# Kernel optimization log

Hardware: AMD Instinct MI355X
Metric: run time of the kernel (lower is better)

Reference implementation:

```python
import jax, jax.numpy as jnp
import numpy as np

N = 50000          # nodes
E = 800000         # edges (before self-loops)
IN_C = 128         # input feature dim
H = 4              # attention heads
C = 32             # channels per head (hidden == out == 32)
G = 64             # graphs in the batch
NEG_SLOPE_ATT = 0.2   # PyG GATConv default negative_slope
NEG_SLOPE_ACT = 0.01  # nn.LeakyReLU default


def setup_inputs() -> dict:
    key = jax.random.key(0)
    ks = jax.random.split(key, 16)
    x = jax.random.normal(ks[0], (N, IN_C), dtype=jnp.float32)
    edge_index = jax.random.randint(ks[1], (2, E), 0, N, dtype=jnp.int64)
    batch = jnp.sort(jax.random.randint(ks[2], (N,), 0, G, dtype=jnp.int64))
    def gat_params(k, din):
        k1, k2, k3 = jax.random.split(k, 3)
        W = jax.random.normal(k1, (din, H * C), dtype=jnp.float32) * (1.0 / np.sqrt(din))
        a_src = jax.random.normal(k2, (H, C), dtype=jnp.float32) * 0.1
        a_dst = jax.random.normal(k3, (H, C), dtype=jnp.float32) * 0.1
        b = jnp.zeros((H * C,), dtype=jnp.float32)
        return W, a_src, a_dst, b
    W1, a_src1, a_dst1, b1 = gat_params(ks[3], IN_C)
    W2, a_src2, a_dst2, b2 = gat_params(ks[4], H * C)
    W3, a_src3, a_dst3, b3 = gat_params(ks[5], H * C)
    return dict(x=x, edge_index=edge_index, batch=batch,
                W1=W1, a_src1=a_src1, a_dst1=a_dst1, b1=b1,
                W2=W2, a_src2=a_src2, a_dst2=a_dst2, b2=b2,
                W3=W3, a_src3=a_src3, a_dst3=a_dst3, b3=b3)


def _gat_conv(x, src, dst, W, a_src, a_dst, b):
    """PyG GATConv (concat=True, negative_slope=0.2); self-loops already in src/dst."""
    n = x.shape[0]
    h = (x @ W).reshape(n, H, C)                      # [N,H,C]
    s = jnp.einsum('nhc,hc->nh', h, a_src)            # [N,H]
    d = jnp.einsum('nhc,hc->nh', h, a_dst)            # [N,H]
    e = jax.nn.leaky_relu(s[src] + d[dst], NEG_SLOPE_ATT)  # [E',H]
    # segment softmax over incoming edges of each destination node
    m = jax.ops.segment_max(e, dst, num_segments=n)   # [N,H]
    ex = jnp.exp(e - m[dst])
    denom = jax.ops.segment_sum(ex, dst, num_segments=n)
    alpha = ex / denom[dst]                           # [E',H]
    msg = h[src] * alpha[..., None]                   # [E',H,C]
    out = jax.ops.segment_sum(msg, dst, num_segments=n).reshape(n, H * C)
    return out + b


def reference(x, edge_index, batch,
              W1, a_src1, a_dst1, b1,
              W2, a_src2, a_dst2, b2,
              W3, a_src3, a_dst3, b3):
    n = x.shape[0]
    # add self-loops (PyG GATConv default add_self_loops=True)
    loop = jnp.arange(n, dtype=edge_index.dtype)
    src = jnp.concatenate([edge_index[0], loop])
    dst = jnp.concatenate([edge_index[1], loop])
    # dropout is identity in eval mode
    h = jax.nn.leaky_relu(_gat_conv(x, src, dst, W1, a_src1, a_dst1, b1), NEG_SLOPE_ACT)
    h = jax.nn.leaky_relu(_gat_conv(h, src, dst, W2, a_src2, a_dst2, b2), NEG_SLOPE_ACT)
    h = jax.nn.leaky_relu(_gat_conv(h, src, dst, W3, a_src3, a_dst3, b3), NEG_SLOPE_ACT)
    graph_embedding = jax.ops.segment_max(h, batch, num_segments=G)  # [G, H*C]
    return (graph_embedding, h, edge_index)
```

## Files before the change

kernel.cpp:

```cpp
#include <hip/hip_runtime.h>
#include <math.h>
#include <limits.h>

#define LRELU_ATT 0.2f
#define LRELU_ACT 0.01f
#define CAP 48
#define ALST (CAP * 4 + 4)
#define DPB 16
#define LCAP 768
#define NBMAX 512
#define TILE 8192
#define BCAP 6528
#define WPAD 136

typedef __attribute__((ext_vector_type(8))) short bf16x8;
typedef __attribute__((ext_vector_type(4))) float f32x4;

__device__ __forceinline__ float lrelu(float x, float s) { return x > 0.f ? x : x * s; }

__device__ __forceinline__ void atomicMaxF(float* addr, float val) {
    int* ai = (int*)addr;
    int old = *(volatile int*)ai;
    while (__int_as_float(old) < val) {
        int assumed = old;
        old = atomicCAS(ai, assumed, __float_as_int(val));
        if (old == assumed) break;
    }
}

__device__ __forceinline__ unsigned short f2bf(float f) {
    union { float f; unsigned u; } v; v.f = f;
    unsigned r = v.u + 0x7FFF + ((v.u >> 16) & 1);
    return (unsigned short)(r >> 16);
}
__device__ __forceinline__ float bf2f(unsigned short u) {
    union { unsigned u; float f; } v; v.u = ((unsigned)u) << 16;
    return v.f;
}
__device__ __forceinline__ float bflo(unsigned u) {
    union { unsigned u; float f; } v; v.u = u << 16;
    return v.f;
}
__device__ __forceinline__ float bfhi(unsigned u) {
    union { unsigned u; float f; } v; v.u = u & 0xffff0000u;
    return v.f;
}

__device__ __forceinline__ int* scan_incl_512(int* a, int* b, int tid, int nthr) {
    int* in = a; int* out = b;
    for (int off = 1; off < 512; off <<= 1) {
        for (int i = tid; i < 512; i += nthr)
            out[i] = in[i] + (i >= off ? in[i - off] : 0);
        __syncthreads();
        int* t = in; in = out; out = t;
    }
    return in;
}

__global__ __launch_bounds__(256) void gemm_k(const float* __restrict__ X,
                                              const float* __restrict__ Wm,
                                              const float* __restrict__ a_src,
                                              const float* __restrict__ a_dst,
                                              unsigned short* __restrict__ Hb,
                                              float* __restrict__ S,
                                              float* __restrict__ D, int n) {
    __shared__ unsigned short sWt[128 * WPAD];
    __shared__ unsigned short sXt[64 * WPAD];
    __shared__ float sa[128], sb[128];
    int tid = threadIdx.x;
    if (tid < 128) { sa[tid] = a_src[tid]; sb[tid] = a_dst[tid]; }
    int row0 = blockIdx.x * 64;
#pragma unroll
    for (int i = 0; i < 16; i++) {
        int idx4 = tid + 256 * i;
        int k = idx4 >> 5;
        int n0 = (idx4 & 31) * 4;
        float4 wv = *(const float4*)&Wm[k * 128 + n0];
        sWt[(n0 + 0) * WPAD + k] = f2bf(wv.x);
        sWt[(n0 + 1) * WPAD + k] = f2bf(wv.y);
        sWt[(n0 + 2) * WPAD + k] = f2bf(wv.z);
        sWt[(n0 + 3) * WPAD + k] = f2bf(wv.w);
    }
#pragma unroll
    for (int i = 0; i < 8; i++) {
        int idx4 = tid + 256 * i;
        int r = idx4 >> 5;
        int koff = (idx4 & 31) * 4;
        int gr = row0 + r;
        float4 xv = make_float4(0.f, 0.f, 0.f, 0.f);
        if (gr < n) xv = *(const float4*)&X[gr * 128 + koff];
        ushort4 xb;
        xb.x = f2bf(xv.x); xb.y = f2bf(xv.y); xb.z = f2bf(xv.z); xb.w = f2bf(xv.w);
        *(ushort4*)&sXt[r * WPAD + koff] = xb;
    }
    __syncthreads();
    int w = tid >> 6, l = tid & 63;
    int lr = l & 15, lk = l >> 4;
    f32x4 acc[8];
#pragma unroll
    for (int ct = 0; ct < 8; ct++) acc[ct] = (f32x4){0.f, 0.f, 0.f, 0.f};
#pragma unroll
    for (int ks = 0; ks < 4; ks++) {
        int kbase = ks * 32 + lk * 8;
        bf16x8 afrag = *(const bf16x8*)&sXt[(w * 16 + lr) * WPAD + kbase];
#pragma unroll
        for (int ct = 0; ct < 8; ct++) {
            bf16x8 bfrag = *(const bf16x8*)&sWt[(ct * 16 + lr) * WPAD + kbase];
            acc[ct] = __builtin_amdgcn_mfma_f32_16x16x32_bf16(afrag, bfrag, acc[ct], 0, 0, 0);
        }
    }
    float sp[4][4], dp[4][4];
#pragma unroll
    for (int reg = 0; reg < 4; reg++) {
#pragma unroll
        for (int hd = 0; hd < 4; hd++) {
            int c0 = (2 * hd) * 16 + lr;
            int c1 = (2 * hd + 1) * 16 + lr;
            sp[reg][hd] = acc[2 * hd][reg] * sa[c0] + acc[2 * hd + 1][reg] * sa[c1];
            dp[reg][hd] = acc[2 * hd][reg] * sb[c0] + acc[2 * hd + 1][reg] * sb[c1];
        }
    }
#pragma unroll
    for (int o = 1; o < 16; o <<= 1) {
#pragma unroll
        for (int reg = 0; reg < 4; reg++) {
#pragma unroll
            for (int hd = 0; hd < 4; hd++) {
                sp[reg][hd] += __shfl_xor(sp[reg][hd], o, 64);
                dp[reg][hd] += __shfl_xor(dp[reg][hd], o, 64);
            }
        }
    }
#pragma unroll
    for (int reg = 0; reg < 4; reg++) {
        int gr = row0 + w * 16 + lk * 4 + reg;
        if (gr < n) {
#pragma unroll
            for (int ct = 0; ct < 8; ct++)
                Hb[gr * 128 + ct * 16 + lr] = f2bf(acc[ct][reg]);
            if (lr == 0) {
                *(float4*)&S[gr * 4] = make_float4(sp[reg][0], sp[reg][1], sp[reg][2], sp[reg][3]);
                *(float4*)&D[gr * 4] = make_float4(dp[reg][0], dp[reg][1], dp[reg][2], dp[reg][3]);
            }
        }
    }
}

__global__ void fill_f_k(float* __restrict__ p, float v, int cnt) {
    int i = blockIdx.x * blockDim.x + threadIdx.x;
    if (i < cnt) p[i] = v;
}
__global__ void fill_i_k(int* __restrict__ p, int v, int cnt) {
    int i = blockIdx.x * blockDim.x + threadIdx.x;
    if (i < cnt) p[i] = v;
}

__global__ void bhist_k(const int* __restrict__ ei, int* __restrict__ bcount, int E) {
    __shared__ int h[NBMAX];
    for (int i = threadIdx.x; i < NBMAX; i += 256) h[i] = 0;
    __syncthreads();
    for (int e = blockIdx.x * blockDim.x + threadIdx.x; e < E; e += gridDim.x * blockDim.x)
        atomicAdd(&h[ei[E + e] >> 7], 1);
    __syncthreads();
    for (int i = threadIdx.x; i < NBMAX; i += 256)
        if (h[i]) atomicAdd(&bcount[i], h[i]);
}

__global__ void bscan_k(const int* __restrict__ bcount, int* __restrict__ bbase,
                        int* __restrict__ cursor, int NB) {
    __shared__ int sa[512], sb[512];
    int tid = threadIdx.x;
    for (int i = tid; i < 512; i += 256) sa[i] = (i < NB) ? bcount[i] : 0;
    __syncthreads();
    int* inc = scan_incl_512(sa, sb, tid, 256);
    for (int i = tid; i < NB; i += 256) {
        int ex = i ? inc[i - 1] : 0;
        bbase[i] = ex;
        cursor[i] = ex;
    }
    if (tid == 0) bbase[NB] = inc[NB - 1];
}

__global__ __launch_bounds__(256) void bin_scatter_k(const int* __restrict__ ei,
                                                     int* __restrict__ cursor,
                                                     unsigned* __restrict__ binned, int E) {
    __shared__ int hist[NBMAX], excl[NBMAX], curl[NBMAX], gbase[NBMAX];
    __shared__ int sa[512], sb[512];
    __shared__ unsigned staged[TILE];
    int tid = threadIdx.x;
    int e0 = blockIdx.x * TILE;
    for (int i = tid; i < NBMAX; i += 256) hist[i] = 0;
    __syncthreads();
    unsigned keys[TILE / 256];
#pragma unroll
    for (int j = 0; j < TILE / 256; j++) {
        int e = e0 + j * 256 + tid;
        if (e < E) {
            unsigned dst = (unsigned)ei[E + e];
            unsigned src = (unsigned)ei[e];
            unsigned k = (dst << 16) | src;
            keys[j] = k;
            atomicAdd(&hist[k >> 23], 1);
        } else keys[j] = 0xFFFFFFFFu;
    }
    __syncthreads();
    for (int i = tid; i < 512; i += 256) sa[i] = hist[i];
    __syncthreads();
    int* inc = scan_incl_512(sa, sb, tid, 256);
    for (int i = tid; i < NBMAX; i += 256) {
        int ex = i ? inc[i - 1] : 0;
        excl[i] = ex;
        curl[i] = ex;
    }
    __syncthreads();
#pragma unroll
    for (int j = 0; j < TILE / 256; j++) {
        unsigned k = keys[j];
        if (k != 0xFFFFFFFFu) {
            int b = k >> 23;
            int p = atomicAdd(&curl[b], 1);
            staged[p] = k;
        }
    }
    __syncthreads();
    for (int i = tid; i < NBMAX; i += 256) {
        int cnt = hist[i];
        if (cnt) gbase[i] = atomicAdd(&cursor[i], cnt);
    }
    __syncthreads();
    int total = inc[511];
    for (int p = tid; p < total; p += 256) {
        unsigned k = staged[p];
        int b = k >> 23;
        binned[gbase[b] + (p - excl[b])] = k;
    }
}

__global__ __launch_bounds__(1024) void bucket_csr_k(const unsigned* __restrict__ binned,
                                                     const int* __restrict__ bbase,
                                                     int* __restrict__ rowptr,
                                                     int* __restrict__ csr,
                                                     int n, int NB) {
    __shared__ int outL[BCAP];
    __shared__ int sa[512], sb[512];
    __shared__ int lbase[129], cur[128];
    int b = blockIdx.x;
    int tid = threadIdx.x;
    int dst0 = b << 7;
    int ndst = min(128, n - dst0);
    int ebase = bbase[b], ecnt = bbase[b + 1] - ebase;
    for (int i = tid; i < 512; i += 1024) sa[i] = (i < ndst) ? 1 : 0;
    __syncthreads();
    for (int p = tid; p < ecnt; p += 1024) {
        int ld = (int)(binned[ebase + p] >> 16) - dst0;
        atomicAdd(&sa[ld], 1);
    }
    __syncthreads();
    int* inc = scan_incl_512(sa, sb, tid, 1024);
    for (int i = tid; i < ndst; i += 1024) {
        int ex = i ? inc[i - 1] : 0;
        lbase[i] = ex;
        cur[i] = ex;
    }
    if (tid == 0) lbase[ndst] = inc[ndst - 1];
    __syncthreads();
    int total = lbase[ndst];
    for (int i = tid; i < ndst; i += 1024) {
        int p = atomicAdd(&cur[i], 1);
        outL[p] = dst0 + i;
    }
    for (int p = tid; p < ecnt; p += 1024) {
        unsigned k = binned[ebase + p];
        int ld = (int)(k >> 16) - dst0;
        int pos = atomicAdd(&cur[ld], 1);
        outL[pos] = (int)(k & 0xFFFFu);
    }
    __syncthreads();
    int w = tid >> 6, lane = tid & 63;
    for (int d = w; d < ndst; d += 16) {
        int st = lbase[d], en = lbase[d + 1];
        int deg = en - st;
        if (deg <= 1) continue;
        if (deg <= 64) {
            int v = (lane < deg) ? outL[st + lane] : INT_MAX;
            int r = 0;
            for (int j = 0; j < deg; j++) {
                int kj = __shfl(v, j, 64);
                r += (kj < v) || (kj == v && j < lane);
            }
            if (lane < deg) outL[st + r] = v;
        } else if (deg <= 128) {
            int v0 = (lane < deg) ? outL[st + lane] : 0;
            int v1 = (64 + lane < deg) ? outL[st + 64 + lane] : 0;
            int r0 = 0, r1 = 0;
            for (int j = 0; j < deg; j++) {
                int kj = outL[st + j];
                r0 += (kj < v0) || (kj == v0 && j < lane);
                r1 += (kj < v1) || (kj == v1 && j < 64 + lane);
            }
            if (lane < deg) outL[st + r0] = v0;
            if (64 + lane < deg) outL[st + r1] = v1;
        } else if (lane == 0) {
            for (int q = st + 1; q < en; q++) {
                int key = outL[q];
                int r = q - 1;
                while (r >= st && outL[r] > key) { outL[r + 1] = outL[r]; r--; }
                outL[r + 1] = key;
            }
        }
    }
    __syncthreads();
    int gb = ebase + dst0;
    for (int p = tid; p < total; p += 1024) csr[gb + p] = outL[p];
    for (int i = tid; i < ndst; i += 1024) rowptr[dst0 + i] = gb + lbase[i];
    if (b == NB - 1 && tid == 0) rowptr[n] = gb + total;
}

__global__ __launch_bounds__(128) void attn_agg_k(const int* __restrict__ rowptr,
                                                  const int* __restrict__ csr,
                                                  const float* __restrict__ S,
                                                  const float* __restrict__ Dv,
                                                  const unsigned short* __restrict__ Hb,
                                                  const float* __restrict__ bias,
                                                  float* __restrict__ Out, int n) {
    __shared__ unsigned short al16[DPB][ALST];
    __shared__ int srcs[LCAP];
    __shared__ float sm[DPB][4], srd[DPB][4], sdv[DPB][4];
    __shared__ int srp[DPB + 1];
    int tid = threadIdx.x;
    int base = blockIdx.x * DPB;
    if (tid <= DPB) {
        int idx = base + tid;
        srp[tid] = rowptr[idx > n ? n : idx];
    }
    __syncthreads();
    int st0 = srp[0];
    int etot = srp[DPB] - st0;
    for (int i = tid; i < etot && i < LCAP; i += 128) srcs[i] = csr[st0 + i];
    __syncthreads();

    {
        int g = tid >> 3;
        int l = tid & 7;
        int dst = base + g;
        if (dst < n) {
            int lst = srp[g] - st0;
            int deg = srp[g + 1] - srp[g];
            float4 dv = *(const float4*)&Dv[dst * 4];
            float4 m = make_float4(-INFINITY, -INFINITY, -INFINITY, -INFINITY);
            for (int pos = l; pos < deg; pos += 8) {
                int idx = lst + pos;
                int src = (idx < LCAP) ? srcs[idx] : csr[st0 + idx];
                float4 sv = *(const float4*)&S[src * 4];
                float4 e;
                e.x = lrelu(sv.x + dv.x, LRELU_ATT);
                e.y = lrelu(sv.y + dv.y, LRELU_ATT);
                e.z = lrelu(sv.z + dv.z, LRELU_ATT);
                e.w = lrelu(sv.w + dv.w, LRELU_ATT);
                if (pos < CAP) {
                    ushort4 eb;
                    eb.x = f2bf(e.x); eb.y = f2bf(e.y); eb.z = f2bf(e.z); eb.w = f2bf(e.w);
                    *(ushort4*)&al16[g][pos * 4] = eb;
                }
                m.x = fmaxf(m.x, e.x); m.y = fmaxf(m.y, e.y);
                m.z = fmaxf(m.z, e.z); m.w = fmaxf(m.w, e.w);
            }
#pragma unroll
            for (int o = 1; o < 8; o <<= 1) {
                m.x = fmaxf(m.x, __shfl_xor(m.x, o, 64));
                m.y = fmaxf(m.y, __shfl_xor(m.y, o, 64));
                m.z = fmaxf(m.z, __shfl_xor(m.z, o, 64));
                m.w = fmaxf(m.w, __shfl_xor(m.w, o, 64));
            }
            float4 den = make_float4(0.f, 0.f, 0.f, 0.f);
            for (int pos = l; pos < deg; pos += 8) {
                float4 e;
                if (pos < CAP) {
                    ushort4 eb = *(const ushort4*)&al16[g][pos * 4];
                    e.x = bf2f(eb.x); e.y = bf2f(eb.y); e.z = bf2f(eb.z); e.w = bf2f(eb.w);
                } else {
                    int idx = lst + pos;
                    int src = (idx < LCAP) ? srcs[idx] : csr[st0 + idx];
                    float4 sv = *(const float4*)&S[src * 4];
                    e.x = lrelu(sv.x + dv.x, LRELU_ATT);
                    e.y = lrelu(sv.y + dv.y, LRELU_ATT);
                    e.z = lrelu(sv.z + dv.z, LRELU_ATT);
                    e.w = lrelu(sv.w + dv.w, LRELU_ATT);
                }
                float4 ex;
                ex.x = __expf(e.x - m.x); ex.y = __expf(e.y - m.y);
                ex.z = __expf(e.z - m.z); ex.w = __expf(e.w - m.w);
                den.x += ex.x; den.y += ex.y; den.z += ex.z; den.w += ex.w;
                if (pos < CAP) {
                    ushort4 xb;
                    xb.x = f2bf(ex.x); xb.y = f2bf(ex.y); xb.z = f2bf(ex.z); xb.w = f2bf(ex.w);
                    *(ushort4*)&al16[g][pos * 4] = xb;
                }
            }
#pragma unroll
            for (int o = 1; o < 8; o <<= 1) {
                den.x += __shfl_xor(den.x, o, 64);
                den.y += __shfl_xor(den.y, o, 64);
                den.z += __shfl_xor(den.z, o, 64);
                den.w += __shfl_xor(den.w, o, 64);
            }
            float4 rd;
            rd.x = 1.f / den.x; rd.y = 1.f / den.y;
            rd.z = 1.f / den.z; rd.w = 1.f / den.w;
            int lim = deg < CAP ? deg : CAP;
            for (int pos = l; pos < lim; pos += 8) {
                ushort4 xb = *(const ushort4*)&al16[g][pos * 4];
                xb.x = f2bf(bf2f(xb.x) * rd.x);
                xb.y = f2bf(bf2f(xb.y) * rd.y);
                xb.z = f2bf(bf2f(xb.z) * rd.z);
                xb.w = f2bf(bf2f(xb.w) * rd.w);
                *(ushort4*)&al16[g][pos * 4] = xb;
            }
            if (l == 0) {
                *(float4*)&sm[g][0] = m;
                *(float4*)&srd[g][0] = rd;
                *(float4*)&sdv[g][0] = dv;
            }
        }
    }
    __syncthreads();

    int w = tid >> 6;
    int lane = tid & 63;
    int s = lane >> 3;
    int p = lane & 7;
    int g2 = w * 8 + s;
    int dst = base + g2;
    if (dst >= n) return;
    int lst = srp[g2] - st0;
    int deg = srp[g2 + 1] - srp[g2];
    int ch0 = p * 16;
    int hd = p >> 1;
    float smh = sm[g2][hd], srdh = srd[g2][hd], sdvh = sdv[g2][hd];
    float4 a0 = make_float4(0.f, 0.f, 0.f, 0.f);
    float4 a1 = make_float4(0.f, 0.f, 0.f, 0.f);
    float4 a2 = make_float4(0.f, 0.f, 0.f, 0.f);
    float4 a3 = make_float4(0.f, 0.f, 0.f, 0.f);
    for (int pos = 0; pos < deg; pos++) {
        int idx = lst + pos;
        int src = (idx < LCAP) ? srcs[idx] : csr[st0 + idx];
        float a;
        if (pos < CAP) a = bf2f(al16[g2][pos * 4 + hd]);
        else a = __expf(lrelu(S[src * 4 + hd] + sdvh, LRELU_ATT) - smh) * srdh;
        uint4 hA = *(const uint4*)&Hb[src * 128 + ch0];
        uint4 hB = *(const uint4*)&Hb[src * 128 + ch0 + 8];
        a0.x = fmaf(a, bflo(hA.x), a0.x);
        a0.y = fmaf(a, bfhi(hA.x), a0.y);
        a0.z = fmaf(a, bflo(hA.y), a0.z);
        a0.w = fmaf(a, bfhi(hA.y), a0.w);
        a1.x = fmaf(a, bflo(hA.z), a1.x);
        a1.y = fmaf(a, bfhi(hA.z), a1.y);
        a1.z = fmaf(a, bflo(hA.w), a1.z);
        a1.w = fmaf(a, bfhi(hA.w), a1.w);
        a2.x = fmaf(a, bflo(hB.x), a2.x);
        a2.y = fmaf(a, bfhi(hB.x), a2.y);
        a2.z = fmaf(a, bflo(hB.y), a2.z);
        a2.w = fmaf(a, bfhi(hB.y), a2.w);
        a3.x = fmaf(a, bflo(hB.z), a3.x);
        a3.y = fmaf(a, bfhi(hB.z), a3.y);
        a3.z = fmaf(a, bflo(hB.w), a3.z);
        a3.w = fmaf(a, bfhi(hB.w), a3.w);
    }
    float4 b0 = *(const float4*)&bias[ch0];
    float4 b1 = *(const float4*)&bias[ch0 + 4];
    float4 b2 = *(const float4*)&bias[ch0 + 8];
    float4 b3 = *(const float4*)&bias[ch0 + 12];
    float4 o0, o1, o2, o3;
    o0.x = lrelu(a0.x + b0.x, LRELU_ACT); o0.y = lrelu(a0.y + b0.y, LRELU_ACT);
    o0.z = lrelu(a0.z + b0.z, LRELU_ACT); o0.w = lrelu(a0.w + b0.w, LRELU_ACT);
    o1.x = lrelu(a1.x + b1.x, LRELU_ACT); o1.y = lrelu(a1.y + b1.y, LRELU_ACT);
    o1.z = lrelu(a1.z + b1.z, LRELU_ACT); o1.w = lrelu(a1.w + b1.w, LRELU_ACT);
    o2.x = lrelu(a2.x + b2.x, LRELU_ACT); o2.y = lrelu(a2.y + b2.y, LRELU_ACT);
    o2.z = lrelu(a2.z + b2.z, LRELU_ACT); o2.w = lrelu(a2.w + b2.w, LRELU_ACT);
    o3.x = lrelu(a3.x + b3.x, LRELU_ACT); o3.y = lrelu(a3.y + b3.y, LRELU_ACT);
    o3.z = lrelu(a3.z + b3.z, LRELU_ACT); o3.w = lrelu(a3.w + b3.w, LRELU_ACT);
    float* op = &Out[(size_t)dst * 128 + ch0];
    *(float4*)&op[0] = o0;
    *(float4*)&op[4] = o1;
    *(float4*)&op[8] = o2;
    *(float4*)&op[12] = o3;
}

__global__ void ge_max_k(const float* __restrict__ Hf, const int* __restrict__ batch,
                         float* __restrict__ ge, int n) {
    int c = threadIdx.x & 127;
    int rh = threadIdx.x >> 7;
    int node0 = blockIdx.x * 128;
    int hi = min(node0 + 128, n);
    int gid = -1;
    float mv = -INFINITY;
    for (int r = node0 + rh; r < hi; r += 2) {
        int g = batch[r];
        if (g != gid) {
            if (gid >= 0) atomicMaxF(&ge[gid * 128 + c], mv);
            gid = g;
            mv = -INFINITY;
        }
        mv = fmaxf(mv, Hf[r * 128 + c]);
    }
    if (gid >= 0) atomicMaxF(&ge[gid * 128 + c], mv);
}

__global__ void ei_copy_k(const int* __restrict__ ei, float* __restrict__ out, int m) {
    int i = (blockIdx.x * blockDim.x + threadIdx.x) * 4;
    if (i + 3 < m) {
        int4 v = *(const int4*)&ei[i];
        float4 o = make_float4((float)v.x, (float)v.y, (float)v.z, (float)v.w);
        *(float4*)&out[i] = o;
    } else {
        for (; i < m; i++) out[i] = (float)ei[i];
    }
}

extern "C" void kernel_launch(void* const* d_in, const int* in_sizes, int n_in,
                              void* d_out, int out_size, void* d_ws, size_t ws_size,
                              hipStream_t stream) {
    const float* x = (const float*)d_in[0];
    const int* ei = (const int*)d_in[1];
    const int* batch = (const int*)d_in[2];
    const float* Wm[3]   = {(const float*)d_in[3], (const float*)d_in[7],  (const float*)d_in[11]};
    const float* asrc[3] = {(const float*)d_in[4], (const float*)d_in[8],  (const float*)d_in[12]};
    const float* adst[3] = {(const float*)d_in[5], (const float*)d_in[9],  (const float*)d_in[13]};
    const float* bias[3] = {(const float*)d_in[6], (const float*)d_in[10], (const float*)d_in[14]};

    const int n = in_sizes[2];
    const int E = in_sizes[1] / 2;
    const int ne = E + n;
    const int G = (out_size - n * 128 - 2 * E) / 128;
    const int NB = (n + 127) >> 7;

    char* w = (char*)d_ws;
    float* Xact = (float*)w;          w += (size_t)n * 128 * 4;
    unsigned short* Hb = (unsigned short*)w; w += (size_t)n * 128 * 2;
    float* S    = (float*)w; w += (size_t)n * 4 * 4;
    float* D    = (float*)w; w += (size_t)n * 4 * 4;
    int* bcount = (int*)w;   w += NBMAX * 4;
    int* bbase  = (int*)w;   w += (NBMAX + 1) * 4;
    int* cursor = (int*)w;   w += NBMAX * 4;
    int* rowptr = (int*)w;   w += (size_t)(n + 1) * 4;
    unsigned* binned = (unsigned*)w; w += (size_t)E * 4;
    int* csr    = (int*)w;   w += (size_t)ne * 4;

    float* out   = (float*)d_out;
    float* ge    = out;
    float* hout  = out + (size_t)G * 128;
    float* eiout = out + (size_t)G * 128 + (size_t)n * 128;

    fill_i_k<<<(NBMAX + 255) / 256, 256, 0, stream>>>(bcount, 0, NBMAX);
    bhist_k<<<256, 256, 0, stream>>>(ei, bcount, E);
    bscan_k<<<1, 256, 0, stream>>>(bcount, bbase, cursor, NB);
    bin_scatter_k<<<(E + TILE - 1) / TILE, 256, 0, stream>>>(ei, cursor, binned, E);
    bucket_csr_k<<<NB, 1024, 0, stream>>>(binned, bbase, rowptr, csr, n, NB);

    const float* xin = x;
    for (int L = 0; L < 3; L++) {
        gemm_k<<<(n + 63) / 64, 256, 0, stream>>>(xin, Wm[L], asrc[L], adst[L], Hb, S, D, n);
        float* xnext = (L == 2) ? hout : Xact;
        attn_agg_k<<<(n + DPB - 1) / DPB, 128, 0, stream>>>(rowptr, csr, S, D, Hb, bias[L], xnext, n);
        xin = xnext;
    }

    fill_f_k<<<(G * 128 + 255) / 256, 256, 0, stream>>>(ge, -INFINITY, G * 128);
    ge_max_k<<<(n + 127) / 128, 256, 0, stream>>>(hout, batch, ge, n);
    ei_copy_k<<<(2 * E / 4 + 255) / 256, 256, 0, stream>>>(ei, eiout, 2 * E);
}
```

Baseline: 299.1 us.

## Unroll aggregation by two edges, vectorize histogram, per-graph max reduction

```diff
diff --git a/kernel.cpp b/kernel.cpp
--- a/kernel.cpp
+++ b/kernel.cpp
@@ -17,16 +17,6 @@
 typedef __attribute__((ext_vector_type(4))) float f32x4;
 
 __device__ __forceinline__ float lrelu(float x, float s) { return x > 0.f ? x : x * s; }
-
-__device__ __forceinline__ void atomicMaxF(float* addr, float val) {
-    int* ai = (int*)addr;
-    int old = *(volatile int*)ai;
-    while (__int_as_float(old) < val) {
-        int assumed = old;
-        old = atomicCAS(ai, assumed, __float_as_int(val));
-        if (old == assumed) break;
-    }
-}
 
 __device__ __forceinline__ unsigned short f2bf(float f) {
     union { float f; unsigned u; } v; v.f = f;
@@ -146,10 +136,6 @@
     }
 }
 
-__global__ void fill_f_k(float* __restrict__ p, float v, int cnt) {
-    int i = blockIdx.x * blockDim.x + threadIdx.x;
-    if (i < cnt) p[i] = v;
-}
 __global__ void fill_i_k(int* __restrict__ p, int v, int cnt) {
     int i = blockIdx.x * blockDim.x + threadIdx.x;
     if (i < cnt) p[i] = v;
@@ -159,7 +145,16 @@
     __shared__ int h[NBMAX];
     for (int i = threadIdx.x; i < NBMAX; i += 256) h[i] = 0;
     __syncthreads();
-    for (int e = blockIdx.x * blockDim.x + threadIdx.x; e < E; e += gridDim.x * blockDim.x)
+    int stride4 = gridDim.x * blockDim.x * 4;
+    for (int e = (blockIdx.x * blockDim.x + threadIdx.x) * 4; e + 3 < E; e += stride4) {
+        int4 d = *(const int4*)&ei[E + e];
+        atomicAdd(&h[d.x >> 7], 1);
+        atomicAdd(&h[d.y >> 7], 1);
+        atomicAdd(&h[d.z >> 7], 1);
+        atomicAdd(&h[d.w >> 7], 1);
+    }
+    int tail0 = E & ~3;
+    for (int e = tail0 + blockIdx.x * blockDim.x + threadIdx.x; e < E; e += gridDim.x * blockDim.x)
         atomicAdd(&h[ei[E + e] >> 7], 1);
     __syncthreads();
     for (int i = threadIdx.x; i < NBMAX; i += 256)
@@ -441,31 +436,60 @@
     float4 a1 = make_float4(0.f, 0.f, 0.f, 0.f);
     float4 a2 = make_float4(0.f, 0.f, 0.f, 0.f);
     float4 a3 = make_float4(0.f, 0.f, 0.f, 0.f);
-    for (int pos = 0; pos < deg; pos++) {
-        int idx = lst + pos;
-        int src = (idx < LCAP) ? srcs[idx] : csr[st0 + idx];
-        float a;
-        if (pos < CAP) a = bf2f(al16[g2][pos * 4 + hd]);
-        else a = __expf(lrelu(S[src * 4 + hd] + sdvh, LRELU_ATT) - smh) * srdh;
-        uint4 hA = *(const uint4*)&Hb[src * 128 + ch0];
-        uint4 hB = *(const uint4*)&Hb[src * 128 + ch0 + 8];
-        a0.x = fmaf(a, bflo(hA.x), a0.x);
-        a0.y = fmaf(a, bfhi(hA.x), a0.y);
-        a0.z = fmaf(a, bflo(hA.y), a0.z);
-        a0.w = fmaf(a, bfhi(hA.y), a0.w);
-        a1.x = fmaf(a, bflo(hA.z), a1.x);
-        a1.y = fmaf(a, bfhi(hA.z), a1.y);
-        a1.z = fmaf(a, bflo(hA.w), a1.z);
-        a1.w = fmaf(a, bfhi(hA.w), a1.w);
-        a2.x = fmaf(a, bflo(hB.x), a2.x);
-        a2.y = fmaf(a, bfhi(hB.x), a2.y);
-        a2.z = fmaf(a, bflo(hB.y), a2.z);
-        a2.w = fmaf(a, bfhi(hB.y), a2.w);
-        a3.x = fmaf(a, bflo(hB.z), a3.x);
-        a3.y = fmaf(a, bfhi(hB.z), a3.y);
-        a3.z = fmaf(a, bflo(hB.w), a3.z);
-        a3.w = fmaf(a, bfhi(hB.w), a3.w);
-    }
+    float4 c0 = make_float4(0.f, 0.f, 0.f, 0.f);
+    float4 c1 = make_float4(0.f, 0.f, 0.f, 0.f);
+    float4 c2 = make_float4(0.f, 0.f, 0.f, 0.f);
+    float4 c3 = make_float4(0.f, 0.f, 0.f, 0.f);
+    int pos = 0;
+    for (; pos + 1 < deg; pos += 2) {
+        int iA = lst + pos, iB = iA + 1;
+        int srcA = (iA < LCAP) ? srcs[iA] : csr[st0 + iA];
+        int srcB = (iB < LCAP) ? srcs[iB] : csr[st0 + iB];
+        float aA = (pos < CAP) ? bf2f(al16[g2][pos * 4 + hd])
+            : __expf(lrelu(S[srcA * 4 + hd] + sdvh, LRELU_ATT) - smh) * srdh;
+        float aB = (pos + 1 < CAP) ? bf2f(al16[g2][(pos + 1) * 4 + hd])
+            : __expf(lrelu(S[srcB * 4 + hd] + sdvh, LRELU_ATT) - smh) * srdh;
+        uint4 hA0 = *(const uint4*)&Hb[srcA * 128 + ch0];
+        uint4 hA1 = *(const uint4*)&Hb[srcA * 128 + ch0 + 8];
+        uint4 hB0 = *(const uint4*)&Hb[srcB * 128 + ch0];
+        uint4 hB1 = *(const uint4*)&Hb[srcB * 128 + ch0 + 8];
+        a0.x = fmaf(aA, bflo(hA0.x), a0.x); a0.y = fmaf(aA, bfhi(hA0.x), a0.y);
+        a0.z = fmaf(aA, bflo(hA0.y), a0.z); a0.w = fmaf(aA, bfhi(hA0.y), a0.w);
+        a1.x = fmaf(aA, bflo(hA0.z), a1.x); a1.y = fmaf(aA, bfhi(hA0.z), a1.y);
+        a1.z = fmaf(aA, bflo(hA0.w), a1.z); a1.w = fmaf(aA, bfhi(hA0.w), a1.w);
+        a2.x = fmaf(aA, bflo(hA1.x), a2.x); a2.y = fmaf(aA, bfhi(hA1.x), a2.y);
+        a2.z = fmaf(aA, bflo(hA1.y), a2.z); a2.w = fmaf(aA, bfhi(hA1.y), a2.w);
+        a3.x = fmaf(aA, bflo(hA1.z), a3.x); a3.y = fmaf(aA, bfhi(hA1.z), a3.y);
+        a3.z = fmaf(aA, bflo(hA1.w), a3.z); a3.w = fmaf(aA, bfhi(hA1.w), a3.w);
+        c0.x = fmaf(aB, bflo(hB0.x), c0.x); c0.y = fmaf(aB, bfhi(hB0.x), c0.y);
+        c0.z = fmaf(aB, bflo(hB0.y), c0.z); c0.w = fmaf(aB, bfhi(hB0.y), c0.w);
+        c1.x = fmaf(aB, bflo(hB0.z), c1.x); c1.y = fmaf(aB, bfhi(hB0.z), c1.y);
+        c1.z = fmaf(aB, bflo(hB0.w), c1.z); c1.w = fmaf(aB, bfhi(hB0.w), c1.w);
+        c2.x = fmaf(aB, bflo(hB1.x), c2.x); c2.y = fmaf(aB, bfhi(hB1.x), c2.y);
+        c2.z = fmaf(aB, bflo(hB1.y), c2.z); c2.w = fmaf(aB, bfhi(hB1.y), c2.w);
+        c3.x = fmaf(aB, bflo(hB1.z), c3.x); c3.y = fmaf(aB, bfhi(hB1.z), c3.y);
+        c3.z = fmaf(aB, bflo(hB1.w), c3.z); c3.w = fmaf(aB, bfhi(hB1.w), c3.w);
+    }
+    if (pos < deg) {
+        int iA = lst + pos;
+        int srcA = (iA < LCAP) ? srcs[iA] : csr[st0 + iA];
+        float aA = (pos < CAP) ? bf2f(al16[g2][pos * 4 + hd])
+            : __expf(lrelu(S[srcA * 4 + hd] + sdvh, LRELU_ATT) - smh) * srdh;
+        uint4 hA0 = *(const uint4*)&Hb[srcA * 128 + ch0];
+        uint4 hA1 = *(const uint4*)&Hb[srcA * 128 + ch0 + 8];
+        a0.x = fmaf(aA, bflo(hA0.x), a0.x); a0.y = fmaf(aA, bfhi(hA0.x), a0.y);
+        a0.z = fmaf(aA, bflo(hA0.y), a0.z); a0.w = fmaf(aA, bfhi(hA0.y), a0.w);
+        a1.x = fmaf(aA, bflo(hA0.z), a1.x); a1.y = fmaf(aA, bfhi(hA0.z), a1.y);
+        a1.z = fmaf(aA, bflo(hA0.w), a1.z); a1.w = fmaf(aA, bfhi(hA0.w), a1.w);
+        a2.x = fmaf(aA, bflo(hA1.x), a2.x); a2.y = fmaf(aA, bfhi(hA1.x), a2.y);
+        a2.z = fmaf(aA, bflo(hA1.y), a2.z); a2.w = fmaf(aA, bfhi(hA1.y), a2.w);
+        a3.x = fmaf(aA, bflo(hA1.z), a3.x); a3.y = fmaf(aA, bfhi(hA1.z), a3.y);
+        a3.z = fmaf(aA, bflo(hA1.w), a3.z); a3.w = fmaf(aA, bfhi(hA1.w), a3.w);
+    }
+    a0.x += c0.x; a0.y += c0.y; a0.z += c0.z; a0.w += c0.w;
+    a1.x += c1.x; a1.y += c1.y; a1.z += c1.z; a1.w += c1.w;
+    a2.x += c2.x; a2.y += c2.y; a2.z += c2.z; a2.w += c2.w;
+    a3.x += c3.x; a3.y += c3.y; a3.z += c3.z; a3.w += c3.w;
     float4 b0 = *(const float4*)&bias[ch0];
     float4 b1 = *(const float4*)&bias[ch0 + 4];
     float4 b2 = *(const float4*)&bias[ch0 + 8];
@@ -486,24 +510,23 @@
     *(float4*)&op[12] = o3;
 }
 
-__global__ void ge_max_k(const float* __restrict__ Hf, const int* __restrict__ batch,
-                         float* __restrict__ ge, int n) {
+__global__ __launch_bounds__(256) void ge_graph_k(const float* __restrict__ Hf,
+                                                  const int* __restrict__ batch,
+                                                  float* __restrict__ ge, int n) {
+    __shared__ float red[256];
+    int g = blockIdx.x;
+    int lo = 0, hi = n;
+    while (lo < hi) { int mid = (lo + hi) >> 1; if (batch[mid] < g) lo = mid + 1; else hi = mid; }
+    int lo2 = lo, hi2 = n;
+    while (lo2 < hi2) { int mid = (lo2 + hi2) >> 1; if (batch[mid] < g + 1) lo2 = mid + 1; else hi2 = mid; }
     int c = threadIdx.x & 127;
     int rh = threadIdx.x >> 7;
-    int node0 = blockIdx.x * 128;
-    int hi = min(node0 + 128, n);
-    int gid = -1;
-    float mv = -INFINITY;
-    for (int r = node0 + rh; r < hi; r += 2) {
-        int g = batch[r];
-        if (g != gid) {
-            if (gid >= 0) atomicMaxF(&ge[gid * 128 + c], mv);
-            gid = g;
-            mv = -INFINITY;
-        }
-        mv = fmaxf(mv, Hf[r * 128 + c]);
-    }
-    if (gid >= 0) atomicMaxF(&ge[gid * 128 + c], mv);
+    float m = -INFINITY;
+    for (int r = lo + rh; r < lo2; r += 2)
+        m = fmaxf(m, Hf[(size_t)r * 128 + c]);
+    red[threadIdx.x] = m;
+    __syncthreads();
+    if (rh == 0) ge[g * 128 + c] = fmaxf(red[c], red[128 + c]);
 }
 
 __global__ void ei_copy_k(const int* __restrict__ ei, float* __restrict__ out, int m) {
@@ -565,7 +588,6 @@
         xin = xnext;
     }
 
-    fill_f_k<<<(G * 128 + 255) / 256, 256, 0, stream>>>(ge, -INFINITY, G * 128);
-    ge_max_k<<<(n + 127) / 128, 256, 0, stream>>>(hout, batch, ge, n);
+    ge_graph_k<<<G, 256, 0, stream>>>(hout, batch, ge, n);
     ei_copy_k<<<(2 * E / 4 + 255) / 256, 256, 0, stream>>>(ei, eiout, 2 * E);
 }
```

Result: slower. 351.8 us (+17.6%).
